# Performance work log

Measured on AMD Instinct MI355X. Metric: run time of the kernel, lower is better.

Reference implementation:

```python
import jax, jax.numpy as jnp
import numpy as np

NUM_HEADS = 16
NUM_EXPERTS = 8
TOP_K = 2
LN_EPS = 1e-5


def _layernorm(x, g, b):
    mu = x.mean(-1, keepdims=True)
    var = ((x - mu) ** 2).mean(-1, keepdims=True)
    return (x - mu) * jax.lax.rsqrt(var + LN_EPS) * g + b


def _rope(x, cos, sin):
    # x: [B,S,H,D]; cos/sin: [S, D//2]; interleaved even/odd pairs
    B, S, H, D = x.shape
    xr = x.reshape(B, S, H, D // 2, 2)
    xe, xo = xr[..., 0], xr[..., 1]
    c = cos[None, :, None, :]
    s = sin[None, :, None, :]
    ye = xe * c - xo * s
    yo = xe * s + xo * c
    return jnp.stack((ye, yo), axis=-1).reshape(B, S, H, D)


def setup_inputs() -> dict:
    key = jax.random.key(0)
    ks = jax.random.split(key, 8)
    B, S, D = 4, 512, 1024
    E, Hd = NUM_EXPERTS, 1792
    sc = 0.02
    return {
        'x': jax.random.normal(ks[0], (B, S, D), jnp.float32),
        'ln1_g': jnp.ones((D,), jnp.float32),
        'ln1_b': jnp.zeros((D,), jnp.float32),
        'ln2_g': jnp.ones((D,), jnp.float32),
        'ln2_b': jnp.zeros((D,), jnp.float32),
        'w_qkv': jax.random.normal(ks[1], (D, 3 * D), jnp.float32) * sc,
        'w_o': jax.random.normal(ks[2], (D, D), jnp.float32) * sc,
        'gate_w': jax.random.normal(ks[3], (D, E), jnp.float32) * sc,
        'w_gate': jax.random.normal(ks[4], (E, D, Hd), jnp.float32) * sc,
        'w_up': jax.random.normal(ks[5], (E, D, Hd), jnp.float32) * sc,
        'w_down': jax.random.normal(ks[6], (E, Hd, D), jnp.float32) * sc,
    }


def reference(x, ln1_g, ln1_b, ln2_g, ln2_b, w_qkv, w_o, gate_w, w_gate, w_up, w_down):
    B, S, D = x.shape
    H = NUM_HEADS
    hd = D // H

    # --- attention with RoPE ---
    xn = _layernorm(x, ln1_g, ln1_b)
    qkv = xn @ w_qkv                      # [B,S,3D]
    q, k, v = jnp.split(qkv, 3, axis=-1)
    q = q.reshape(B, S, H, hd)
    k = k.reshape(B, S, H, hd)
    v = v.reshape(B, S, H, hd)
    inv_freq = 1.0 / (10000.0 ** (jnp.arange(0, hd, 2, dtype=jnp.float32) / hd))
    t = jnp.arange(S, dtype=jnp.float32)
    freqs = jnp.outer(t, inv_freq)        # [S, hd//2]
    cos, sin = jnp.cos(freqs), jnp.sin(freqs)
    q = _rope(q, cos, sin)
    k = _rope(k, cos, sin)
    scale = 1.0 / jnp.sqrt(jnp.asarray(hd, x.dtype))
    scores = jnp.einsum('bshd,bthd->bhst', q, k) * scale
    causal = jnp.tril(jnp.ones((S, S), bool))
    scores = jnp.where(causal[None, None], scores, jnp.finfo(scores.dtype).min)
    attn = jax.nn.softmax(scores, axis=-1)
    attn_out = jnp.einsum('bhst,bthd->bshd', attn, v).reshape(B, S, D)
    x = x + attn_out @ w_o

    # --- MoE ---
    xn2 = _layernorm(x, ln2_g, ln2_b)
    xf = xn2.reshape(-1, D)               # [T, D]
    logits = (xf.astype(jnp.bfloat16) @ gate_w.astype(jnp.bfloat16)).astype(jnp.float32)
    topk_w, topk_i = jax.lax.top_k(logits, TOP_K)
    topk_w = jax.nn.softmax(topk_w, axis=-1)
    probs = jax.nn.softmax(logits, axis=-1)
    expert_dist = probs.mean(0)
    lb_loss = NUM_EXPERTS * (expert_dist ** 2).sum()
    # dense dispatch: combine weights [T,E], zero where not selected (same math as sort/gather/scatter)
    cw = (jax.nn.one_hot(topk_i, NUM_EXPERTS, dtype=xf.dtype) * topk_w[..., None].astype(xf.dtype)).sum(1)
    g = jnp.einsum('td,edh->teh', xf, w_gate)
    u = jnp.einsum('td,edh->teh', xf, w_up)
    h = jax.nn.silu(g) * u
    down = jnp.einsum('teh,ehd->ted', h, w_down)
    moe_out = jnp.einsum('ted,te->td', down, cw).reshape(B, S, D)
    x = x + moe_out
    return (x, lb_loss, expert_dist)
```

## Files before the change

kernel.cpp:

```cpp
#include <hip/hip_runtime.h>
#include <hip/hip_bf16.h>
#include <math.h>

#define B_    4
#define S_    512
#define D_    1024
#define T_    2048
#define H_    16
#define HD_   64
#define E_    8
#define HID_  1792
#define D3_   3072
#define GU_   (2 * HID_)
#define NPART_ 72

typedef unsigned short ushort_t;
typedef __bf16 bf16x8 __attribute__((ext_vector_type(8)));
typedef float  floatx4 __attribute__((ext_vector_type(4)));

__constant__ int kPrefix[16] = {0,1,2,4,6,9,12,16,20,25,30,36,42,49,56,64};

__device__ inline float bf2f(ushort_t u) {
    return __uint_as_float(((unsigned)u) << 16);
}
__device__ inline ushort_t f2bf(float f) {
    __hip_bfloat16 h = __float2bfloat16(f);
    return __builtin_bit_cast(ushort_t, h);
}

__device__ __forceinline__ void gl2lds16(const ushort_t* g, ushort_t* l) {
    __builtin_amdgcn_global_load_lds(
        (const __attribute__((address_space(1))) void*)g,
        (__attribute__((address_space(3))) void*)l, 16, 0, 0);
}

__global__ __launch_bounds__(256) void transpose_bf16_kernel(
    const float* __restrict__ in, ushort_t* __restrict__ out,
    int R, int C, int mul, int add, long outEstride)
{
    __shared__ float tile[32][33];
    const int bx = blockIdx.x * 32;
    const int by = blockIdx.y * 32;
    const size_t iofs = (size_t)blockIdx.z * R * C;
    const size_t oofs = (size_t)blockIdx.z * outEstride;
    const int tx = threadIdx.x & 31;
    const int ty = threadIdx.x >> 5;
#pragma unroll
    for (int i = 0; i < 4; i++) {
        int r = by + ty + i * 8;
        tile[ty + i * 8][tx] = in[iofs + (size_t)r * C + bx + tx];
    }
    __syncthreads();
#pragma unroll
    for (int i = 0; i < 4; i++) {
        int c = bx + ty + i * 8;
        out[oofs + (size_t)(c * mul + add) * R + by + tx] = f2bf(tile[tx][ty + i * 8]);
    }
}

__global__ __launch_bounds__(256) void ln_kernel(
    const float* __restrict__ x, const float* __restrict__ g,
    const float* __restrict__ b, float* __restrict__ outf,
    ushort_t* __restrict__ outb)
{
    const int t = blockIdx.x;
    const int tid = threadIdx.x;
    const int wave = tid >> 6, lane = tid & 63;
    const float4 v = ((const float4*)(x + (size_t)t * D_))[tid];

    float s = v.x + v.y + v.z + v.w;
#pragma unroll
    for (int off = 32; off; off >>= 1) s += __shfl_xor(s, off);
    __shared__ float red1[4];
    __shared__ float red2[4];
    if (lane == 0) red1[wave] = s;
    __syncthreads();
    const float mu = (red1[0] + red1[1] + red1[2] + red1[3]) * (1.0f / D_);

    const float dx = v.x - mu, dy = v.y - mu, dz = v.z - mu, dw = v.w - mu;
    float vs = dx * dx + dy * dy + dz * dz + dw * dw;
#pragma unroll
    for (int off = 32; off; off >>= 1) vs += __shfl_xor(vs, off);
    if (lane == 0) red2[wave] = vs;
    __syncthreads();
    const float var = (red2[0] + red2[1] + red2[2] + red2[3]) * (1.0f / D_);
    const float rs = 1.0f / sqrtf(var + 1e-5f);

    const float4 gg = ((const float4*)g)[tid];
    const float4 bb = ((const float4*)b)[tid];
    float4 o;
    o.x = dx * rs * gg.x + bb.x;
    o.y = dy * rs * gg.y + bb.y;
    o.z = dz * rs * gg.z + bb.z;
    o.w = dw * rs * gg.w + bb.w;
    if (outf) ((float4*)(outf + (size_t)t * D_))[tid] = o;
    if (outb) {
        ushort4 ob;
        ob.x = f2bf(o.x); ob.y = f2bf(o.y); ob.z = f2bf(o.z); ob.w = f2bf(o.w);
        ((ushort4*)(outb + (size_t)t * D_))[tid] = ob;
    }
}

template<int TM>
__global__ __launch_bounds__(256) void sgemm_kernel(
    const float* __restrict__ A, const float* __restrict__ B,
    const float* __restrict__ res, float* __restrict__ C,
    float* __restrict__ C2, int M, int N, int K)
{
    constexpr int RM  = TM / 16;
    constexpr int TPR = 256 / TM;
    constexpr int KF  = 16 / TPR;
    __shared__ float As[16][TM + 4];
    __shared__ float Bs[16][68];
    const int tid = threadIdx.x;
    const int m0 = blockIdx.y * TM, n0 = blockIdx.x * 64;
    const int tx = tid & 15, ty = tid >> 4;

    float acc[RM][4] = {};

    const int arow = tid / TPR;
    const int akk  = (tid % TPR) * KF;
    const int bk = tid >> 4;
    const int bc = (tid & 15) * 4;

    const float* Ap = A + (size_t)(m0 + arow) * K + akk;
    const float* Bp = B + (size_t)bk * N + n0 + bc;

    for (int k0 = 0; k0 < K; k0 += 16) {
        float av[KF];
#pragma unroll
        for (int f = 0; f < KF / 4; f++) {
            const float4 t = *(const float4*)(Ap + k0 + f * 4);
            av[f * 4 + 0] = t.x; av[f * 4 + 1] = t.y;
            av[f * 4 + 2] = t.z; av[f * 4 + 3] = t.w;
        }
        const float4 bv = *(const float4*)(Bp + (size_t)k0 * N);
        __syncthreads();
#pragma unroll
        for (int i = 0; i < KF; i++) As[akk + i][arow] = av[i];
        *(float4*)&Bs[bk][bc] = bv;
        __syncthreads();
#pragma unroll
        for (int k = 0; k < 16; k++) {
            float a[RM];
#pragma unroll
            for (int f = 0; f < RM / 4; f++) {
                const float4 t = *(const float4*)&As[k][ty * RM + f * 4];
                a[f * 4 + 0] = t.x; a[f * 4 + 1] = t.y;
                a[f * 4 + 2] = t.z; a[f * 4 + 3] = t.w;
            }
            const float4 bb = *(const float4*)&Bs[k][tx * 4];
            const float bj[4] = {bb.x, bb.y, bb.z, bb.w};
#pragma unroll
            for (int i = 0; i < RM; i++)
#pragma unroll
                for (int j = 0; j < 4; j++)
                    acc[i][j] = fmaf(a[i], bj[j], acc[i][j]);
        }
    }

#pragma unroll
    for (int i = 0; i < RM; i++) {
        const int row = m0 + ty * RM + i;
        const size_t base = (size_t)row * N + n0 + tx * 4;
        float4 o;
        o.x = acc[i][0]; o.y = acc[i][1]; o.z = acc[i][2]; o.w = acc[i][3];
        if (res) {
            const float4 r0 = *(const float4*)(res + base);
            o.x += r0.x; o.y += r0.y; o.z += r0.z; o.w += r0.w;
        }
        *(float4*)(C + base) = o;
        if (C2) *(float4*)(C2 + base) = o;
    }
}

__global__ __launch_bounds__(256) void gateup_idx_kernel(
    const ushort_t* __restrict__ A, const ushort_t* __restrict__ Bgu,
    const int* __restrict__ cnt, const int* __restrict__ tok,
    ushort_t* __restrict__ Hc)
{
    const int e = blockIdx.z;
    const int cntE = cnt[e];
    const int row0 = blockIdx.y * 128;
    if (row0 >= cntE) return;
    const int col0 = blockIdx.x * 128;
    const ushort_t* Bt = Bgu + (size_t)e * GU_ * D_;
    ushort_t* Hp = Hc + (size_t)e * T_ * HID_;

    __shared__ __align__(16) ushort_t As[128 * 32];
    __shared__ __align__(16) ushort_t Bs[128 * 32];
    const int tid = threadIdx.x, w = tid >> 6, lane = tid & 63;
    const int lr = lane >> 2, lc = (lane & 3) * 8;
    const int wm = (w >> 1) * 64, wn = (w & 1) * 64;
    const int lm = lane & 15, lq = lane >> 4;

    floatx4 acc[4][4] = {};

    int r0c = row0 + w * 16 + lr;  if (r0c > cntE - 1) r0c = cntE - 1;
    int r1c = row0 + 64 + w * 16 + lr; if (r1c > cntE - 1) r1c = cntE - 1;
    const ushort_t* Ap0 = A + (size_t)tok[e * T_ + r0c] * D_ + lc;
    const ushort_t* Ap1 = A + (size_t)tok[e * T_ + r1c] * D_ + lc;
    const ushort_t* Bp = Bt + (size_t)(col0 + w * 16 + lr) * D_ + lc;
    ushort_t* lA = As + w * 512;
    ushort_t* lB = Bs + w * 512;

    for (int k0 = 0; k0 < D_; k0 += 32) {
        __syncthreads();
        gl2lds16(Ap0 + k0, lA);
        gl2lds16(Ap1 + k0, lA + 2048);
        gl2lds16(Bp + k0, lB);
        gl2lds16(Bp + k0 + (size_t)64 * D_, lB + 2048);
        __syncthreads();
        bf16x8 a[4], b[4];
#pragma unroll
        for (int i = 0; i < 4; i++)
            a[i] = *(const bf16x8*)(As + (wm + i * 16 + lm) * 32 + lq * 8);
#pragma unroll
        for (int j = 0; j < 4; j++)
            b[j] = *(const bf16x8*)(Bs + (wn + j * 16 + lm) * 32 + lq * 8);
#pragma unroll
        for (int i = 0; i < 4; i++)
#pragma unroll
            for (int j = 0; j < 4; j++)
                acc[i][j] = __builtin_amdgcn_mfma_f32_16x16x32_bf16(a[i], b[j], acc[i][j], 0, 0, 0);
    }

#pragma unroll
    for (int i = 0; i < 4; i++)
#pragma unroll
        for (int j = 0; j < 4; j++)
#pragma unroll
            for (int r = 0; r < 4; r++) {
                const float v = acc[i][j][r];
                const float vp = __shfl_xor(v, 1);
                const float g = (lm & 1) ? vp : v;
                const float u = (lm & 1) ? v : vp;
                const float h = g / (1.f + __expf(-g)) * u;
                if (!(lm & 1)) {
                    const int row = row0 + wm + i * 16 + lq * 4 + r;
                    const int col = col0 + wn + j * 16 + lm;
                    Hp[(size_t)row * HID_ + (col >> 1)] = f2bf(h);
                }
            }
}

__global__ __launch_bounds__(256) void down_idx_kernel(
    const ushort_t* __restrict__ Hc, const ushort_t* __restrict__ Wd,
    const int* __restrict__ cnt, const int* __restrict__ tok,
    const float* __restrict__ wt, float* __restrict__ out)
{
    const int e = blockIdx.z;
    const int cntE = cnt[e];
    const int row0 = blockIdx.y * 128;
    if (row0 >= cntE) return;
    const int col0 = blockIdx.x * 128;
    const ushort_t* A = Hc + (size_t)e * T_ * HID_;
    const ushort_t* Bt = Wd + (size_t)e * D_ * HID_;

    __shared__ __align__(16) ushort_t As[128 * 32];
    __shared__ __align__(16) ushort_t Bs[128 * 32];
    const int tid = threadIdx.x, w = tid >> 6, lane = tid & 63;
    const int lr = lane >> 2, lc = (lane & 3) * 8;
    const int wm = (w >> 1) * 64, wn = (w & 1) * 64;
    const int lm = lane & 15, lq = lane >> 4;

    floatx4 acc[4][4] = {};

    const ushort_t* Ap = A + (size_t)(row0 + w * 16 + lr) * HID_ + lc;
    const ushort_t* Bp = Bt + (size_t)(col0 + w * 16 + lr) * HID_ + lc;
    ushort_t* lA = As + w * 512;
    ushort_t* lB = Bs + w * 512;

    for (int k0 = 0; k0 < HID_; k0 += 32) {
        __syncthreads();
        gl2lds16(Ap + k0, lA);
        gl2lds16(Ap + k0 + (size_t)64 * HID_, lA + 2048);
        gl2lds16(Bp + k0, lB);
        gl2lds16(Bp + k0 + (size_t)64 * HID_, lB + 2048);
        __syncthreads();
        bf16x8 a[4], b[4];
#pragma unroll
        for (int i = 0; i < 4; i++)
            a[i] = *(const bf16x8*)(As + (wm + i * 16 + lm) * 32 + lq * 8);
#pragma unroll
        for (int j = 0; j < 4; j++)
            b[j] = *(const bf16x8*)(Bs + (wn + j * 16 + lm) * 32 + lq * 8);
#pragma unroll
        for (int i = 0; i < 4; i++)
#pragma unroll
            for (int j = 0; j < 4; j++)
                acc[i][j] = __builtin_amdgcn_mfma_f32_16x16x32_bf16(a[i], b[j], acc[i][j], 0, 0, 0);
    }

#pragma unroll
    for (int i = 0; i < 4; i++)
#pragma unroll
        for (int r = 0; r < 4; r++) {
            const int row = row0 + wm + i * 16 + lq * 4 + r;
            if (row < cntE) {
                const int t = tok[e * T_ + row];
                const float scale = wt[e * T_ + row];
#pragma unroll
                for (int j = 0; j < 4; j++) {
                    const int col = col0 + wn + j * 16 + lm;
                    atomicAdd(&out[(size_t)t * D_ + col], scale * acc[i][j][r]);
                }
            }
        }
}

__global__ __launch_bounds__(256) void rope_table_kernel(
    float* __restrict__ ctab, float* __restrict__ stab)
{
    const int i = blockIdx.x * 256 + threadIdx.x;
    if (i >= S_ * 32) return;
    const int s = i >> 5, p = i & 31;
    const double e = (double)(2 * p) / 64.0;
    const float pf = (float)pow(10000.0, e);
    const float invf = 1.0f / pf;
    const float fr = (float)s * invf;
    ctab[i] = (float)cos((double)fr);
    stab[i] = (float)sin((double)fr);
}

__global__ __launch_bounds__(256) void rope_kernel(
    float* __restrict__ qkv, const float* __restrict__ ctab,
    const float* __restrict__ stab)
{
    const int n = blockIdx.x * 256 + threadIdx.x;
    const int pair = n & 31;
    const int h = (n >> 5) & 15;
    const int t = n >> 9;
    const int s = t & (S_ - 1);
    const float c = ctab[s * 32 + pair];
    const float sn = stab[s * 32 + pair];
    const size_t base = (size_t)t * D3_ + h * HD_ + pair * 2;
    float x0 = qkv[base], x1 = qkv[base + 1];
    qkv[base]     = x0 * c - x1 * sn;
    qkv[base + 1] = x0 * sn + x1 * c;
    x0 = qkv[base + D_]; x1 = qkv[base + D_ + 1];
    qkv[base + D_]     = x0 * c - x1 * sn;
    qkv[base + D_ + 1] = x0 * sn + x1 * c;
}

__global__ __launch_bounds__(256) void attn_part_kernel(
    const float* __restrict__ qkv, float* __restrict__ Opart,
    float* __restrict__ Ml)
{
    const int qt = blockIdx.y;
    const int kc = blockIdx.x;
    if (kc > (qt >> 1)) return;
    const int bh = blockIdx.z;
    const int b = bh >> 4, h = bh & 15;
    const int q0 = qt * 32;
    const int c0 = kc * 64;
    const int pidx = bh * NPART_ + kPrefix[qt] + kc;

    __shared__ __align__(16) float kbuf[64][68];
    __shared__ __align__(16) float vbuf[64][68];
    __shared__ __align__(16) float qs[32][68];
    __shared__ __align__(16) float ps[4][8][68];

    const int tid = threadIdx.x, wave = tid >> 6, lane = tid & 63;

    for (int i = tid; i < 32 * 16; i += 256) {
        const int qi = i >> 4, g = i & 15;
        const int t = b * S_ + q0 + qi;
        *(float4*)&qs[qi][g * 4] =
            *(const float4*)(qkv + (size_t)t * D3_ + h * HD_ + g * 4);
    }
    for (int i = tid; i < 64 * 16; i += 256) {
        const int key = i >> 4, g = i & 15;
        const int t = b * S_ + c0 + key;
        *(float4*)&kbuf[key][g * 4] =
            *(const float4*)(qkv + (size_t)t * D3_ + D_ + h * HD_ + g * 4);
        *(float4*)&vbuf[key][g * 4] =
            *(const float4*)(qkv + (size_t)t * D3_ + 2 * D_ + h * HD_ + g * 4);
    }
    __syncthreads();

    const int kglob = c0 + lane;
    float sc[8];
#pragma unroll
    for (int qi = 0; qi < 8; qi++) sc[qi] = 0.f;
#pragma unroll 4
    for (int g = 0; g < 16; g++) {
        const float4 kv = *(const float4*)&kbuf[lane][g * 4];
#pragma unroll
        for (int qi = 0; qi < 8; qi++) {
            const float4 qv = *(const float4*)&qs[wave * 8 + qi][g * 4];
            float s = sc[qi];
            s = fmaf(qv.x, kv.x, s);
            s = fmaf(qv.y, kv.y, s);
            s = fmaf(qv.z, kv.z, s);
            s = fmaf(qv.w, kv.w, s);
            sc[qi] = s;
        }
    }
#pragma unroll
    for (int qi = 0; qi < 8; qi++) {
        const int s = q0 + wave * 8 + qi;
        float v = (kglob <= s) ? sc[qi] * 0.125f : -INFINITY;
        float cmax = v;
#pragma unroll
        for (int off = 32; off; off >>= 1) cmax = fmaxf(cmax, __shfl_xor(cmax, off));
        const float p = (v == -INFINITY) ? 0.f : expf(v - cmax);
        float psum = p;
#pragma unroll
        for (int off = 32; off; off >>= 1) psum += __shfl_xor(psum, off);
        ps[wave][qi][lane] = p;
        if (lane == 0) {
            Ml[(size_t)pidx * 64 + wave * 8 + qi] = cmax;
            Ml[(size_t)pidx * 64 + 32 + wave * 8 + qi] = psum;
        }
    }

    float O[8];
#pragma unroll
    for (int qi = 0; qi < 8; qi++) O[qi] = 0.f;
#pragma unroll 4
    for (int g = 0; g < 16; g++) {
        const float v0 = vbuf[g * 4 + 0][lane];
        const float v1 = vbuf[g * 4 + 1][lane];
        const float v2 = vbuf[g * 4 + 2][lane];
        const float v3 = vbuf[g * 4 + 3][lane];
#pragma unroll
        for (int qi = 0; qi < 8; qi++) {
            const float4 p4 = *(const float4*)&ps[wave][qi][g * 4];
            float o = O[qi];
            o = fmaf(p4.x, v0, o);
            o = fmaf(p4.y, v1, o);
            o = fmaf(p4.z, v2, o);
            o = fmaf(p4.w, v3, o);
            O[qi] = o;
        }
    }
#pragma unroll
    for (int qi = 0; qi < 8; qi++)
        Opart[((size_t)pidx * 32 + wave * 8 + qi) * 64 + lane] = O[qi];
}

__global__ __launch_bounds__(256) void attn_combine_kernel(
    const float* __restrict__ Opart, const float* __restrict__ Ml,
    float* __restrict__ out)
{
    const int qt = blockIdx.x, bh = blockIdx.y;
    const int b = bh >> 4, h = bh & 15;
    const int nchunk = (qt >> 1) + 1;
    const int base = bh * NPART_ + kPrefix[qt];
    const int tid = threadIdx.x;
    const int qrow = tid >> 3;
    const int d0 = (tid & 7) * 8;

    float M = -INFINITY;
    for (int c = 0; c < nchunk; c++)
        M = fmaxf(M, Ml[(size_t)(base + c) * 64 + qrow]);

    float L = 0.f;
    float o[8] = {0, 0, 0, 0, 0, 0, 0, 0};
    for (int c = 0; c < nchunk; c++) {
        const float mc = Ml[(size_t)(base + c) * 64 + qrow];
        const float lc = Ml[(size_t)(base + c) * 64 + 32 + qrow];
        const float w = (mc == -INFINITY) ? 0.f : expf(mc - M);
        L = fmaf(lc, w, L);
        const size_t ob = ((size_t)(base + c) * 32 + qrow) * 64 + d0;
        const float4 a0 = *(const float4*)(Opart + ob);
        const float4 a1 = *(const float4*)(Opart + ob + 4);
        o[0] = fmaf(a0.x, w, o[0]); o[1] = fmaf(a0.y, w, o[1]);
        o[2] = fmaf(a0.z, w, o[2]); o[3] = fmaf(a0.w, w, o[3]);
        o[4] = fmaf(a1.x, w, o[4]); o[5] = fmaf(a1.y, w, o[5]);
        o[6] = fmaf(a1.z, w, o[6]); o[7] = fmaf(a1.w, w, o[7]);
    }
    const float inv = 1.f / L;
    const int t = b * S_ + qt * 32 + qrow;
    float4 r0, r1;
    r0.x = o[0] * inv; r0.y = o[1] * inv; r0.z = o[2] * inv; r0.w = o[3] * inv;
    r1.x = o[4] * inv; r1.y = o[5] * inv; r1.z = o[6] * inv; r1.w = o[7] * inv;
    *(float4*)(out + (size_t)t * D_ + h * HD_ + d0) = r0;
    *(float4*)(out + (size_t)t * D_ + h * HD_ + d0 + 4) = r1;
}

__global__ __launch_bounds__(64) void gate_kernel(
    const ushort_t* __restrict__ xn2, const float* __restrict__ gate_w,
    int* __restrict__ cnt, int* __restrict__ tok, float* __restrict__ wt,
    float* __restrict__ probs)
{
    const int t = blockIdx.x;
    const int lane = threadIdx.x;
    float acc[8] = {0, 0, 0, 0, 0, 0, 0, 0};
    for (int d = lane; d < D_; d += 64) {
        const float xv = bf2f(xn2[(size_t)t * D_ + d]);
        const float4 g0 = ((const float4*)(gate_w + d * 8))[0];
        const float4 g1 = ((const float4*)(gate_w + d * 8))[1];
        acc[0] = fmaf(xv, bf2f(f2bf(g0.x)), acc[0]);
        acc[1] = fmaf(xv, bf2f(f2bf(g0.y)), acc[1]);
        acc[2] = fmaf(xv, bf2f(f2bf(g0.z)), acc[2]);
        acc[3] = fmaf(xv, bf2f(f2bf(g0.w)), acc[3]);
        acc[4] = fmaf(xv, bf2f(f2bf(g1.x)), acc[4]);
        acc[5] = fmaf(xv, bf2f(f2bf(g1.y)), acc[5]);
        acc[6] = fmaf(xv, bf2f(f2bf(g1.z)), acc[6]);
        acc[7] = fmaf(xv, bf2f(f2bf(g1.w)), acc[7]);
    }
#pragma unroll
    for (int e = 0; e < 8; e++) {
#pragma unroll
        for (int off = 32; off; off >>= 1) acc[e] += __shfl_xor(acc[e], off);
        acc[e] = bf2f(f2bf(acc[e]));
    }

    if (lane == 0) {
        int i1 = 0;
        for (int e = 1; e < 8; e++) if (acc[e] > acc[i1]) i1 = e;
        int i2 = (i1 == 0) ? 1 : 0;
        for (int e = 0; e < 8; e++) if (e != i1 && acc[e] > acc[i2]) i2 = e;
        const float e2 = expf(acc[i2] - acc[i1]);
        const float w1 = 1.f / (1.f + e2);
        const float w2 = e2 * w1;
        const int p1 = atomicAdd(&cnt[i1], 1);
        tok[i1 * T_ + p1] = t; wt[i1 * T_ + p1] = w1;
        const int p2 = atomicAdd(&cnt[i2], 1);
        tok[i2 * T_ + p2] = t; wt[i2 * T_ + p2] = w2;
        const float mx = acc[i1];
        float se = 0.f, pe[8];
        for (int e = 0; e < 8; e++) { pe[e] = expf(acc[e] - mx); se += pe[e]; }
        const float inv = 1.f / se;
        for (int e = 0; e < 8; e++) probs[t * 8 + e] = pe[e] * inv;
    }
}

__global__ void zero_route_kernel(int* __restrict__ cnt)
{
    if (threadIdx.x < 8) cnt[threadIdx.x] = 0;
}

__global__ __launch_bounds__(256) void reduce_dist_kernel(
    const float* __restrict__ probs, float* __restrict__ out)
{
    __shared__ float part[256];
    __shared__ float dist8[8];
    const int tid = threadIdx.x;
    const int e = tid & 7, chunk = tid >> 3;
    float s = 0.f;
    for (int t = chunk; t < T_; t += 32) s += probs[t * 8 + e];
    part[tid] = s;
    __syncthreads();
    if (tid < 8) {
        float tot = 0.f;
        for (int c = 0; c < 32; c++) tot += part[c * 8 + tid];
        const float dv = tot * (1.0f / T_);
        dist8[tid] = dv;
        out[(size_t)T_ * D_ + 1 + tid] = dv;
    }
    __syncthreads();
    if (tid == 0) {
        float s2 = 0.f;
        for (int k = 0; k < 8; k++) s2 += dist8[k] * dist8[k];
        out[(size_t)T_ * D_] = (float)E_ * s2;
    }
}

extern "C" void kernel_launch(void* const* d_in, const int* in_sizes, int n_in,
                              void* d_out, int out_size, void* d_ws, size_t ws_size,
                              hipStream_t stream)
{
    const float* x      = (const float*)d_in[0];
    const float* ln1_g  = (const float*)d_in[1];
    const float* ln1_b  = (const float*)d_in[2];
    const float* ln2_g  = (const float*)d_in[3];
    const float* ln2_b  = (const float*)d_in[4];
    const float* w_qkv  = (const float*)d_in[5];
    const float* w_o    = (const float*)d_in[6];
    const float* gate_w = (const float*)d_in[7];
    const float* w_gate = (const float*)d_in[8];
    const float* w_up   = (const float*)d_in[9];
    const float* w_down = (const float*)d_in[10];
    float* out = (float*)d_out;

    char* ws = (char*)d_ws;
    size_t off = 0;
    auto alloc = [&](size_t bytes) { size_t o = off; off += (bytes + 255) & ~(size_t)255; return o; };
    ushort_t* wguT  = (ushort_t*)(ws + alloc((size_t)E_ * GU_ * D_ * 2));
    ushort_t* wdT   = (ushort_t*)(ws + alloc((size_t)E_ * D_ * HID_ * 2));
    float*    xn    = (float*)   (ws + alloc((size_t)T_ * D_ * 4));
    ushort_t* xn2   = (ushort_t*)(ws + alloc((size_t)T_ * D_ * 2));
    int*      cnt   = (int*)     (ws + alloc(64));
    int*      tok   = (int*)     (ws + alloc((size_t)E_ * T_ * 4));
    float*    wt    = (float*)   (ws + alloc((size_t)E_ * T_ * 4));
    float*    probs = (float*)   (ws + alloc((size_t)T_ * E_ * 4));
    float*    ctab  = (float*)   (ws + alloc((size_t)S_ * 32 * 4));
    float*    stab  = (float*)   (ws + alloc((size_t)S_ * 32 * 4));
    const size_t qkvBytes   = (size_t)T_ * D3_ * 4;
    const size_t opartBytes = (size_t)64 * NPART_ * 32 * 64 * 4;
    const size_t mlBytes    = (size_t)64 * NPART_ * 64 * 4;
    const size_t scratch0 = alloc(qkvBytes + opartBytes + mlBytes);
    float*    qkv   = (float*)   (ws + scratch0);
    float*    Opart = (float*)   (ws + scratch0 + qkvBytes);
    float*    Ml    = (float*)   (ws + scratch0 + qkvBytes + opartBytes);
    float*    attnO = (float*)   (ws + scratch0);
    float*    x1    = (float*)   (ws + scratch0 + (size_t)T_ * D_ * 4);
    ushort_t* Hc    = (ushort_t*)(ws + scratch0);
    (void)ws_size; (void)in_sizes; (void)n_in; (void)out_size;

    hipLaunchKernelGGL(transpose_bf16_kernel, dim3(HID_ / 32, D_ / 32, E_), dim3(256), 0, stream,
                       w_gate, wguT, D_, HID_, 2, 0, (long)GU_ * D_);
    hipLaunchKernelGGL(transpose_bf16_kernel, dim3(HID_ / 32, D_ / 32, E_), dim3(256), 0, stream,
                       w_up, wguT, D_, HID_, 2, 1, (long)GU_ * D_);
    hipLaunchKernelGGL(transpose_bf16_kernel, dim3(D_ / 32, HID_ / 32, E_), dim3(256), 0, stream,
                       w_down, wdT, HID_, D_, 1, 0, (long)D_ * HID_);

    hipLaunchKernelGGL(rope_table_kernel, dim3((S_ * 32 + 255) / 256), dim3(256), 0, stream,
                       ctab, stab);

    hipLaunchKernelGGL(ln_kernel, dim3(T_), dim3(256), 0, stream,
                       x, ln1_g, ln1_b, xn, (ushort_t*)nullptr);

    hipLaunchKernelGGL((sgemm_kernel<128>), dim3(D3_ / 64, T_ / 128), dim3(256), 0, stream,
                       xn, w_qkv, (const float*)nullptr, qkv, (float*)nullptr, T_, D3_, D_);

    hipLaunchKernelGGL(rope_kernel, dim3(T_ * H_ * 32 / 256), dim3(256), 0, stream,
                       qkv, ctab, stab);

    hipLaunchKernelGGL(attn_part_kernel, dim3(8, 16, 64), dim3(256), 0, stream,
                       qkv, Opart, Ml);
    hipLaunchKernelGGL(attn_combine_kernel, dim3(16, 64), dim3(256), 0, stream,
                       Opart, Ml, attnO);

    hipLaunchKernelGGL((sgemm_kernel<64>), dim3(D_ / 64, T_ / 64), dim3(256), 0, stream,
                       attnO, w_o, x, x1, out, T_, D_, D_);

    hipLaunchKernelGGL(ln_kernel, dim3(T_), dim3(256), 0, stream,
                       x1, ln2_g, ln2_b, (float*)nullptr, xn2);

    hipLaunchKernelGGL(zero_route_kernel, dim3(1), dim3(64), 0, stream, cnt);
    hipLaunchKernelGGL(gate_kernel, dim3(T_), dim3(64), 0, stream,
                       xn2, gate_w, cnt, tok, wt, probs);
    hipLaunchKernelGGL(reduce_dist_kernel, dim3(1), dim3(256), 0, stream, probs, out);

    hipLaunchKernelGGL(gateup_idx_kernel, dim3(GU_ / 128, T_ / 128, E_), dim3(256), 0, stream,
                       xn2, wguT, cnt, tok, Hc);
    hipLaunchKernelGGL(down_idx_kernel, dim3(D_ / 128, T_ / 128, E_), dim3(256), 0, stream,
                       Hc, wdT, cnt, tok, wt, out);
}
```

Baseline: 841.8 us.

## Split-K the QKV projection and MoE down GEMM, fuse partial-sum add with RoPE

The QKV sgemm is split into two K halves, each writing its own partial buffer, and a new kernel sums the two partials and applies RoPE to the Q/K columns in one pass, which replaces the old standalone rope kernel. The MoE down-projection grid is doubled along z so each block handles half of the hidden dimension, with results still combined through atomicAdd into the output. The aim is more blocks in flight on the many CUs of the device. The cost is extra partial-buffer traffic, more atomics on the output, and reuse of the Opart scratch region for the second partial, which is safe only because attention runs afterwards.

```diff
diff --git a/kernel.cpp b/kernel.cpp
--- a/kernel.cpp
+++ b/kernel.cpp
@@ -174,6 +174,97 @@
     }
 }
 
+__global__ __launch_bounds__(256) void sgemm_splitk_kernel(
+    const float* __restrict__ A, const float* __restrict__ B,
+    float* __restrict__ Cpart, int M, int N, int K, int KS)
+{
+    __shared__ float As[16][132];
+    __shared__ float Bs[16][68];
+    const int tid = threadIdx.x;
+    const int m0 = blockIdx.y * 128, n0 = blockIdx.x * 64;
+    const int z = blockIdx.z;
+    const int kBegin = z * KS;
+    const int tx = tid & 15, ty = tid >> 4;
+
+    float acc[8][4] = {};
+
+    const int arow = tid >> 1;
+    const int akk  = (tid & 1) * 8;
+    const int bk = tid >> 4;
+    const int bc = (tid & 15) * 4;
+
+    const float* Ap = A + (size_t)(m0 + arow) * K + kBegin + akk;
+    const float* Bp = B + (size_t)(kBegin + bk) * N + n0 + bc;
+
+    for (int k0 = 0; k0 < KS; k0 += 16) {
+        float av[8];
+#pragma unroll
+        for (int f = 0; f < 2; f++) {
+            const float4 t = *(const float4*)(Ap + k0 + f * 4);
+            av[f * 4 + 0] = t.x; av[f * 4 + 1] = t.y;
+            av[f * 4 + 2] = t.z; av[f * 4 + 3] = t.w;
+        }
+        const float4 bv = *(const float4*)(Bp + (size_t)k0 * N);
+        __syncthreads();
+#pragma unroll
+        for (int i = 0; i < 8; i++) As[akk + i][arow] = av[i];
+        *(float4*)&Bs[bk][bc] = bv;
+        __syncthreads();
+#pragma unroll
+        for (int k = 0; k < 16; k++) {
+            float a[8];
+#pragma unroll
+            for (int f = 0; f < 2; f++) {
+                const float4 t = *(const float4*)&As[k][ty * 8 + f * 4];
+                a[f * 4 + 0] = t.x; a[f * 4 + 1] = t.y;
+                a[f * 4 + 2] = t.z; a[f * 4 + 3] = t.w;
+            }
+            const float4 bb = *(const float4*)&Bs[k][tx * 4];
+            const float bj[4] = {bb.x, bb.y, bb.z, bb.w};
+#pragma unroll
+            for (int i = 0; i < 8; i++)
+#pragma unroll
+                for (int j = 0; j < 4; j++)
+                    acc[i][j] = fmaf(a[i], bj[j], acc[i][j]);
+        }
+    }
+
+    float* Cz = Cpart + (size_t)z * M * N;
+#pragma unroll
+    for (int i = 0; i < 8; i++) {
+        const int row = m0 + ty * 8 + i;
+        const size_t base = (size_t)row * N + n0 + tx * 4;
+        float4 o;
+        o.x = acc[i][0]; o.y = acc[i][1]; o.z = acc[i][2]; o.w = acc[i][3];
+        *(float4*)(Cz + base) = o;
+    }
+}
+
+__global__ __launch_bounds__(256) void rope_add_kernel(
+    float* __restrict__ P0, const float* __restrict__ P1,
+    const float* __restrict__ ctab, const float* __restrict__ stab)
+{
+    const int t = blockIdx.y;
+    const int c2 = blockIdx.x * 256 + threadIdx.x;
+    const int col = c2 * 2;
+    const size_t idx = (size_t)t * D3_ + col;
+    const float2 a0 = *(const float2*)(P0 + idx);
+    const float2 a1 = *(const float2*)(P1 + idx);
+    float x0 = a0.x + a1.x;
+    float x1 = a0.y + a1.y;
+    if (col < 2 * D_) {
+        const int pair = (col & 63) >> 1;
+        const int s = t & (S_ - 1);
+        const float c = ctab[s * 32 + pair];
+        const float sn = stab[s * 32 + pair];
+        const float y0 = x0 * c - x1 * sn;
+        const float y1 = x0 * sn + x1 * c;
+        x0 = y0; x1 = y1;
+    }
+    float2 o; o.x = x0; o.y = x1;
+    *(float2*)(P0 + idx) = o;
+}
+
 __global__ __launch_bounds__(256) void gateup_idx_kernel(
     const ushort_t* __restrict__ A, const ushort_t* __restrict__ Bgu,
     const int* __restrict__ cnt, const int* __restrict__ tok,
@@ -249,11 +340,13 @@
     const int* __restrict__ cnt, const int* __restrict__ tok,
     const float* __restrict__ wt, float* __restrict__ out)
 {
-    const int e = blockIdx.z;
+    const int e = blockIdx.z >> 1;
+    const int ks = blockIdx.z & 1;
     const int cntE = cnt[e];
     const int row0 = blockIdx.y * 128;
     if (row0 >= cntE) return;
     const int col0 = blockIdx.x * 128;
+    const int kBegin = ks * (HID_ / 2);
     const ushort_t* A = Hc + (size_t)e * T_ * HID_;
     const ushort_t* Bt = Wd + (size_t)e * D_ * HID_;
 
@@ -266,12 +359,12 @@
 
     floatx4 acc[4][4] = {};
 
-    const ushort_t* Ap = A + (size_t)(row0 + w * 16 + lr) * HID_ + lc;
-    const ushort_t* Bp = Bt + (size_t)(col0 + w * 16 + lr) * HID_ + lc;
+    const ushort_t* Ap = A + (size_t)(row0 + w * 16 + lr) * HID_ + kBegin + lc;
+    const ushort_t* Bp = Bt + (size_t)(col0 + w * 16 + lr) * HID_ + kBegin + lc;
     ushort_t* lA = As + w * 512;
     ushort_t* lB = Bs + w * 512;
 
-    for (int k0 = 0; k0 < HID_; k0 += 32) {
+    for (int k0 = 0; k0 < HID_ / 2; k0 += 32) {
         __syncthreads();
         gl2lds16(Ap + k0, lA);
         gl2lds16(Ap + k0 + (size_t)64 * HID_, lA + 2048);
@@ -321,26 +414,6 @@
     const float fr = (float)s * invf;
     ctab[i] = (float)cos((double)fr);
     stab[i] = (float)sin((double)fr);
-}
-
-__global__ __launch_bounds__(256) void rope_kernel(
-    float* __restrict__ qkv, const float* __restrict__ ctab,
-    const float* __restrict__ stab)
-{
-    const int n = blockIdx.x * 256 + threadIdx.x;
-    const int pair = n & 31;
-    const int h = (n >> 5) & 15;
-    const int t = n >> 9;
-    const int s = t & (S_ - 1);
-    const float c = ctab[s * 32 + pair];
-    const float sn = stab[s * 32 + pair];
-    const size_t base = (size_t)t * D3_ + h * HD_ + pair * 2;
-    float x0 = qkv[base], x1 = qkv[base + 1];
-    qkv[base]     = x0 * c - x1 * sn;
-    qkv[base + 1] = x0 * sn + x1 * c;
-    x0 = qkv[base + D_]; x1 = qkv[base + D_ + 1];
-    qkv[base + D_]     = x0 * c - x1 * sn;
-    qkv[base + D_ + 1] = x0 * sn + x1 * c;
 }
 
 __global__ __launch_bounds__(256) void attn_part_kernel(
@@ -593,7 +666,8 @@
     const size_t opartBytes = (size_t)64 * NPART_ * 32 * 64 * 4;
     const size_t mlBytes    = (size_t)64 * NPART_ * 64 * 4;
     const size_t scratch0 = alloc(qkvBytes + opartBytes + mlBytes);
-    float*    qkv   = (float*)   (ws + scratch0);
+    float*    qkvP0 = (float*)   (ws + scratch0);
+    float*    qkvP1 = (float*)   (ws + scratch0 + qkvBytes);
     float*    Opart = (float*)   (ws + scratch0 + qkvBytes);
     float*    Ml    = (float*)   (ws + scratch0 + qkvBytes + opartBytes);
     float*    attnO = (float*)   (ws + scratch0);
@@ -614,14 +688,14 @@
     hipLaunchKernelGGL(ln_kernel, dim3(T_), dim3(256), 0, stream,
                        x, ln1_g, ln1_b, xn, (ushort_t*)nullptr);
 
-    hipLaunchKernelGGL((sgemm_kernel<128>), dim3(D3_ / 64, T_ / 128), dim3(256), 0, stream,
-                       xn, w_qkv, (const float*)nullptr, qkv, (float*)nullptr, T_, D3_, D_);
-
-    hipLaunchKernelGGL(rope_kernel, dim3(T_ * H_ * 32 / 256), dim3(256), 0, stream,
-                       qkv, ctab, stab);
+    hipLaunchKernelGGL(sgemm_splitk_kernel, dim3(D3_ / 64, T_ / 128, 2), dim3(256), 0, stream,
+                       xn, w_qkv, qkvP0, T_, D3_, D_, D_ / 2);
+
+    hipLaunchKernelGGL(rope_add_kernel, dim3(6, T_), dim3(256), 0, stream,
+                       qkvP0, qkvP1, ctab, stab);
 
     hipLaunchKernelGGL(attn_part_kernel, dim3(8, 16, 64), dim3(256), 0, stream,
-                       qkv, Opart, Ml);
+                       qkvP0, Opart, Ml);
     hipLaunchKernelGGL(attn_combine_kernel, dim3(16, 64), dim3(256), 0, stream,
                        Opart, Ml, attnO);
 
@@ -638,6 +712,6 @@
 
     hipLaunchKernelGGL(gateup_idx_kernel, dim3(GU_ / 128, T_ / 128, E_), dim3(256), 0, stream,
                        xn2, wguT, cnt, tok, Hc);
-    hipLaunchKernelGGL(down_idx_kernel, dim3(D_ / 128, T_ / 128, E_), dim3(256), 0, stream,
+    hipLaunchKernelGGL(down_idx_kernel, dim3(D_ / 128, T_ / 128, E_ * 2), dim3(256), 0, stream,
                        Hc, wdT, cnt, tok, wt, out);
 }
```

New measurement: 827.1 us. Within noise of the previous version (-1.7%).
